# Kernel tuning notes

Hardware: AMD Instinct MI355X
Metric: run time of the kernel (lower is better)

Reference implementation:

```python
import jax, jax.numpy as jnp
import numpy as np

B, DIN, DOUT, E = 131072, 512, 512, 16


def setup_inputs() -> dict:
    key = jax.random.key(0)
    k_x, k_wg, k_we = jax.random.split(key, 3)
    x = jax.random.normal(k_x, (B, DIN), dtype=jnp.float32)
    # gating network params
    Wg = jax.random.normal(k_wg, (DIN, E), dtype=jnp.float32) * 0.02
    bg = jnp.zeros((E,), dtype=jnp.float32)
    # GRN params (torch inits them to zero -> GRN is identity at init)
    gamma = jnp.zeros((E,), dtype=jnp.float32)
    beta = jnp.zeros((E,), dtype=jnp.float32)
    # per-expert linear params, stacked [E, DIN, DOUT]
    We = jax.random.normal(k_we, (E, DIN, DOUT), dtype=jnp.float32) * 0.02
    be = jnp.zeros((E, DOUT), dtype=jnp.float32)
    return {"x": x, "Wg": Wg, "bg": bg, "gamma": gamma, "beta": beta,
            "We": We, "be": be, "topk": 2}


def reference(x, Wg, bg, gamma, beta, We, be, topk):
    # ---- gating: linear -> GRN over expert dim -> softmax ----
    logits = x @ Wg + bg                                   # [B, E]
    Gx = jnp.linalg.norm(logits, axis=1, keepdims=True)    # [B, 1] L2 over experts
    Nx = Gx / (jnp.mean(Gx, axis=0, keepdims=True) + 1e-6) # [B, 1]
    logits = gamma * (logits * Nx) + beta + logits         # GRN residual
    gates = jax.nn.softmax(logits, axis=-1)                # [B, E]
    # ---- top-k routing ----
    top_vals, top_idx = jax.lax.top_k(gates, topk)         # [B, k]
    n_tok = x.shape[0]
    # combine weights scattered back to dense [B, E] (zero for unrouted experts)
    w = jnp.zeros_like(gates).at[jnp.arange(n_tok)[:, None], top_idx].add(top_vals)
    # ---- per-expert linear + weighted combine ----
    out = jnp.zeros((n_tok, We.shape[-1]), dtype=x.dtype)
    for e in range(We.shape[0]):  # small fixed loop over experts
        out = out + w[:, e:e + 1] * (x @ We[e] + be[e])
    return out
```

## Files before the change

kernel.cpp:

```cpp
#include <hip/hip_runtime.h>
#include <hip/hip_bf16.h>
#include <stdint.h>

#define NTOK 131072
#define NE 16

typedef __attribute__((ext_vector_type(8))) short short8;
typedef __attribute__((ext_vector_type(4))) float f32x4;

#define AS1 __attribute__((address_space(1)))
#define AS3 __attribute__((address_space(3)))

__device__ __forceinline__ ushort f2bf(float f) {
    __hip_bfloat16 h = __float2bfloat16(f);
    return *reinterpret_cast<ushort*>(&h);
}


__global__ void k_init(int* ctrl) {
    int tid = threadIdx.x;
    if (tid < 144) ctrl[tid] = 0;
}

__global__ __launch_bounds__(256) void k_wet(const float* __restrict__ We, ushort* __restrict__ WeT) {
    __shared__ float t[64][65];
    int e = blockIdx.z, k0 = blockIdx.x * 64, n0 = blockIdx.y * 64;
    int tid = threadIdx.x;
    const float* src = We + ((size_t)e * 512 + k0) * 512 + n0;
    #pragma unroll
    for (int i = 0; i < 16; i++) {
        int idx = i * 256 + tid;
        int r = idx >> 6, c = idx & 63;
        t[r][c] = src[(size_t)r * 512 + c];
    }
    __syncthreads();
    ushort* dst = WeT + ((size_t)e * 512 + n0) * 512 + k0;
    #pragma unroll
    for (int i = 0; i < 16; i++) {
        int idx = i * 256 + tid;
        int rn = idx >> 6, ck = idx & 63;
        dst[(size_t)rn * 512 + ck] = f2bf(t[ck][rn]);
    }
}

__global__ __launch_bounds__(256) void k_gate(const float* __restrict__ x, const float* __restrict__ Wg,
                                              const float* __restrict__ bg, float* __restrict__ logits,
                                              float* __restrict__ partials, ushort* __restrict__ xbf) {
    __shared__ float WgL[512 * 16];
    __shared__ float xs[256][33];
    __shared__ float wsum[4];
    const int tid = threadIdx.x;
    #pragma unroll
    for (int i = 0; i < 32; i++) WgL[i * 256 + tid] = Wg[i * 256 + tid];
    const size_t tokBase = (size_t)blockIdx.x * 256;
    float acc[16];
    #pragma unroll
    for (int e = 0; e < 16; e++) acc[e] = 0.f;

    for (int kc = 0; kc < 16; kc++) {
        __syncthreads();
        #pragma unroll
        for (int i = 0; i < 8; i++) {
            int idx = (i << 8) + tid;
            int rr = idx >> 3, cq = (idx & 7) << 2;
            const float4 v = *(const float4*)&x[(tokBase + rr) * 512 + (kc << 5) + cq];
            xs[rr][cq] = v.x; xs[rr][cq + 1] = v.y; xs[rr][cq + 2] = v.z; xs[rr][cq + 3] = v.w;
            if (xbf) {
                ushort4 uw;
                uw.x = f2bf(v.x); uw.y = f2bf(v.y); uw.z = f2bf(v.z); uw.w = f2bf(v.w);
                *(ushort4*)&xbf[(tokBase + rr) * 512 + (kc << 5) + cq] = uw;
            }
        }
        __syncthreads();
        #pragma unroll
        for (int j = 0; j < 32; j++) {
            float xv = xs[tid][j];
            const float* wr = &WgL[((kc << 5) + j) << 4];
            #pragma unroll
            for (int e = 0; e < 16; e++) acc[e] = fmaf(xv, wr[e], acc[e]);
        }
    }

    float lg[16];
    float ss = 0.f;
    #pragma unroll
    for (int e = 0; e < 16; e++) {
        float v = acc[e] + bg[e];
        lg[e] = v;
        ss += v * v;
    }
    float gx = sqrtf(ss);
    float r = gx;
    #pragma unroll
    for (int off = 32; off >= 1; off >>= 1) r += __shfl_down(r, off);
    if ((tid & 63) == 0) wsum[tid >> 6] = r;
    __syncthreads();
    if (tid == 0) partials[blockIdx.x] = wsum[0] + wsum[1] + wsum[2] + wsum[3];
    float4* lo = (float4*)(logits + (tokBase + tid) * 16);
    lo[0] = make_float4(lg[0], lg[1], lg[2], lg[3]);
    lo[1] = make_float4(lg[4], lg[5], lg[6], lg[7]);
    lo[2] = make_float4(lg[8], lg[9], lg[10], lg[11]);
    lo[3] = make_float4(lg[12], lg[13], lg[14], lg[15]);
}

__global__ void k_redsum(const float* __restrict__ partials, float* __restrict__ sumGx) {
    int tid = threadIdx.x;
    float s = 0.f;
    #pragma unroll
    for (int i = 0; i < 8; i++) s += partials[tid + i * 64];
    #pragma unroll
    for (int off = 32; off >= 1; off >>= 1) s += __shfl_down(s, off);
    if (tid == 0) *sumGx = s;
}

__global__ __launch_bounds__(256) void k_route(const float* __restrict__ logits, const float* __restrict__ gamma,
                                               const float* __restrict__ beta, const float* __restrict__ sumGx,
                                               int* __restrict__ eP, float2* __restrict__ wP,
                                               int* __restrict__ cnts, int* __restrict__ blockHist) {
    __shared__ int h[32];
    int tid = threadIdx.x;
    if (tid < 32) h[tid] = 0;
    __syncthreads();
    float mean = sumGx[0] * (1.0f / 131072.0f);
    float inv_mean = 1.0f / (mean + 1e-6f);
    #pragma unroll
    for (int it = 0; it < 4; it++) {
        size_t t = (size_t)blockIdx.x * 1024 + it * 256 + tid;
        const float4* lr = (const float4*)(logits + t * 16);
        float4 a0 = lr[0], a1 = lr[1], a2 = lr[2], a3 = lr[3];
        float lg[16] = {a0.x, a0.y, a0.z, a0.w, a1.x, a1.y, a1.z, a1.w,
                        a2.x, a2.y, a2.z, a2.w, a3.x, a3.y, a3.z, a3.w};
        float ss = 0.f;
        #pragma unroll
        for (int e = 0; e < 16; e++) ss += lg[e] * lg[e];
        float nx = sqrtf(ss) * inv_mean;
        #pragma unroll
        for (int e = 0; e < 16; e++) lg[e] = gamma[e] * (lg[e] * nx) + beta[e] + lg[e];
        int e1 = 0; float v1 = lg[0];
        #pragma unroll
        for (int e = 1; e < 16; e++) if (lg[e] > v1) { v1 = lg[e]; e1 = e; }
        int e2 = -1; float v2 = -3.4e38f;
        #pragma unroll
        for (int e = 0; e < 16; e++) if (e != e1 && lg[e] > v2) { v2 = lg[e]; e2 = e; }
        float s = 0.f;
        #pragma unroll
        for (int e = 0; e < 16; e++) s += expf(lg[e] - v1);
        float w1 = 1.0f / s;
        float w2 = expf(v2 - v1) / s;
        eP[t] = e1 | (e2 << 8);
        wP[t] = make_float2(w1, w2);
        atomicAdd(&h[e1], 1);
        atomicAdd(&h[16 + e2], 1);
    }
    __syncthreads();
    if (tid < 32) {
        atomicAdd(&cnts[tid], h[tid]);
        blockHist[blockIdx.x * 32 + tid] = h[tid];
    }
}

__global__ void k_scan(int* ctrl, int* blockHist) {
    int t = threadIdx.x;
    if (t < 32) {
        int run = 0;
        for (int b = 0; b < 128; b++) {
            int v = blockHist[b * 32 + t];
            blockHist[b * 32 + t] = run;
            run += v;
        }
    }
    __syncthreads();
    if (t == 0) {
        int s = 0;
        for (int e = 0; e < 16; e++) { ctrl[64 + e] = s; s += ctrl[e]; }
        s = 0;
        for (int e = 0; e < 16; e++) { ctrl[80 + e] = s; s += ctrl[16 + e]; }
        int tt = 0; ctrl[96] = 0;
        for (int e = 0; e < 16; e++) { tt += (ctrl[e] + 63) >> 6; ctrl[96 + e + 1] = tt; }
        tt = 0; ctrl[113] = 0;
        for (int e = 0; e < 16; e++) { tt += (ctrl[16 + e] + 63) >> 6; ctrl[113 + e + 1] = tt; }
    }
}

__global__ __launch_bounds__(256) void k_scatter(const int* __restrict__ eP, const float2* __restrict__ wP,
                                                 const int* __restrict__ ctrl, const int* __restrict__ blockHist,
                                                 int* __restrict__ listA, float* __restrict__ wA,
                                                 int* __restrict__ listB, float* __restrict__ wB) {
    __shared__ int waveCnt[4][32];
    __shared__ int runCnt[32];
    const int tid = threadIdx.x;
    const int lane = tid & 63;
    const int wv = tid >> 6;
    if (tid < 32) runCnt[tid] = blockHist[blockIdx.x * 32 + tid];
    __syncthreads();
    const unsigned long long below = (1ull << lane) - 1ull;
    for (int it = 0; it < 4; it++) {
        size_t t = (size_t)blockIdx.x * 1024 + it * 256 + tid;
        int ep = eP[t];
        float2 w = wP[t];
        int e1 = ep & 255, e2 = (ep >> 8) & 255;
        int r1 = 0, r2 = 0;
        for (int e = 0; e < 16; e++) {
            unsigned long long m1 = __ballot(e1 == e);
            unsigned long long m2 = __ballot(e2 == e);
            if (e1 == e) r1 = __popcll(m1 & below);
            if (e2 == e) r2 = __popcll(m2 & below);
            if (lane == e) {
                waveCnt[wv][e] = __popcll(m1);
                waveCnt[wv][16 + e] = __popcll(m2);
            }
        }
        __syncthreads();
        if (tid < 32) {
            int s = runCnt[tid];
            #pragma unroll
            for (int ww = 0; ww < 4; ww++) { int v = waveCnt[ww][tid]; waveCnt[ww][tid] = s; s += v; }
            runCnt[tid] = s;
        }
        __syncthreads();
        int i1 = ctrl[64 + e1] + waveCnt[wv][e1] + r1;
        listA[i1] = (int)t; wA[i1] = w.x;
        int i2 = ctrl[80 + e2] + waveCnt[wv][16 + e2] + r2;
        listB[i2] = (int)t; wB[i2] = w.y;
        __syncthreads();
    }
}

template <int ADD, int ABF>
__global__ __launch_bounds__(256, 3) void k_gemm(const float* __restrict__ x, const ushort* __restrict__ xbf,
                                                 const ushort* __restrict__ WeT,
                                                 const float* __restrict__ be,
                                                 const int* __restrict__ list, const float* __restrict__ wlist,
                                                 const int* __restrict__ cnts, const int* __restrict__ offs,
                                                 const int* __restrict__ tileOff,
                                                 float* __restrict__ out) {
    __shared__ ushort lds[20480];
    const int tid = threadIdx.x;
    const int q = (int)gridDim.x >> 3;
    const int bid = ((int)blockIdx.x & 7) * q + ((int)blockIdx.x >> 3);
    const int ry = bid >> 1;
    const int nh = bid & 1;
    if (ry >= tileOff[16]) return;
    int e = 0;
    #pragma unroll
    for (int i = 1; i < 16; i++) if (ry >= tileOff[i]) e = i;
    const int cnt = cnts[e];
    const int off = offs[e];
    const int rowStart = (ry - tileOff[e]) << 6;
    const int n0 = nh << 8;

    const int sRow = tid >> 2, sQ = tid & 3;
    const int gRow = rowStart + sRow;
    const int tokS = (gRow < cnt) ? list[off + gRow] : 0;
    const float* xrowF = x + (size_t)tokS * 512 + sQ * 16;
    const ushort* xrowH = xbf + (size_t)tokS * 512 + sQ * 16;
    const int aswz = (sRow & 7) << 4;
    const int awr0 = 32768 + sRow * 128;

    const char* weB = (const char*)WeT + (size_t)e * 524288 + (size_t)n0 * 1024;

    const int lane = tid & 63;
    const int wid = tid >> 6;
    const int wN = wid << 6;
    const int l16 = lane & 15;
    const int lq = lane >> 4;
    const int mswz = (l16 & 7) << 4;
    const int kbL = lq << 4;

    f32x4 acc[4][4];
    f32x4 zero = {0.f, 0.f, 0.f, 0.f};
    #pragma unroll
    for (int i = 0; i < 4; i++)
        #pragma unroll
        for (int j = 0; j < 4; j++) acc[i][j] = zero;

    auto stageB = [&](int kt) {
        #pragma unroll
        for (int i = 0; i < 8; i++) {
            int D = (tid << 4) + (i << 12);
            int nr = D >> 7, inner = D & 127;
            int sb = inner ^ ((nr & 7) << 4);
            const char* gp = weB + nr * 1024 + kt * 128 + sb;
            __builtin_amdgcn_global_load_lds((const AS1 void*)gp, (AS3 void*)&lds[D >> 1], 16, 0, 0);
        }
    };
    float4 vaF[4];
    short8 vaH[2];
    auto loadA = [&](int kt) {
        if (ABF) {
            const short8* xp = (const short8*)(xrowH + kt * 64);
            vaH[0] = xp[0]; vaH[1] = xp[1];
        } else {
            const float4* xp = (const float4*)(xrowF + kt * 64);
            #pragma unroll
            for (int j = 0; j < 4; j++) vaF[j] = xp[j];
        }
    };
    auto writeA = [&]() {
        #pragma unroll
        for (int h = 0; h < 2; h++) {
            int db = awr0 + (((sQ << 5) + (h << 4)) ^ aswz);
            if (ABF) {
                *(short8*)((char*)lds + db) = vaH[h];
            } else {
                alignas(16) ushort tw[8];
                float4 p = vaF[h * 2], q2 = vaF[h * 2 + 1];
                tw[0] = f2bf(p.x); tw[1] = f2bf(p.y); tw[2] = f2bf(p.z); tw[3] = f2bf(p.w);
                tw[4] = f2bf(q2.x); tw[5] = f2bf(q2.y); tw[6] = f2bf(q2.z); tw[7] = f2bf(q2.w);
                *(short8*)((char*)lds + db) = *(const short8*)tw;
            }
        }
    };
    auto compute = [&]() {
        #pragma unroll
        for (int ks = 0; ks < 2; ks++) {
            const int kb = (ks << 6) + kbL;
            short8 af[4], bfr[4];
            #pragma unroll
            for (int mf = 0; mf < 4; mf++) {
                int m = (mf << 4) + l16;
                af[mf] = *(const short8*)((const char*)lds + 32768 + (m << 7) + (kb ^ mswz));
            }
            #pragma unroll
            for (int nf = 0; nf < 4; nf++) {
                int n = wN + (nf << 4) + l16;
                bfr[nf] = *(const short8*)((const char*)lds + (n << 7) + (kb ^ mswz));
            }
            #pragma unroll
            for (int mf = 0; mf < 4; mf++)
                #pragma unroll
                for (int nf = 0; nf < 4; nf++)
                    acc[mf][nf] = __builtin_amdgcn_mfma_f32_16x16x32_bf16(af[mf], bfr[nf], acc[mf][nf], 0, 0, 0);
        }
    };

    loadA(0);
    #pragma unroll
    for (int kt = 0; kt < 8; kt++) {
        __syncthreads();
        stageB(kt);
        writeA();
        if (kt < 7) loadA(kt + 1);
        __syncthreads();
        compute();
    }

    float bias[4];
    #pragma unroll
    for (int nf = 0; nf < 4; nf++) bias[nf] = be[e * 512 + n0 + wN + (nf << 4) + l16];
    float* lsf = (float*)lds;
    __syncthreads();
    #pragma unroll
    for (int mf = 0; mf < 4; mf++) {
        int rb = rowStart + (mf << 4) + (lq << 2);
        #pragma unroll
        for (int i = 0; i < 4; i++) {
            int r = rb + i;
            float wv_ = (r < cnt) ? wlist[off + r] : 0.f;
            int lrow = (lq << 2) + i;
            #pragma unroll
            for (int nf = 0; nf < 4; nf++)
                lsf[lrow * 260 + wN + (nf << 4) + l16] = wv_ * (acc[mf][nf][i] + bias[nf]);
        }
        __syncthreads();
        {
            int lrow = tid >> 4, seg = tid & 15;
            int r = rowStart + (mf << 4) + lrow;
            if (r < cnt) {
                int tok = list[off + r];
                float* orow = out + (size_t)tok * 512 + n0;
                #pragma unroll
                for (int j = 0; j < 4; j++) {
                    int c = (seg << 2) + (j << 6);
                    float4 v = *(float4*)&lsf[lrow * 260 + c];
                    if (ADD) {
                        float4 o = *(const float4*)&orow[c];
                        v.x += o.x; v.y += o.y; v.z += o.z; v.w += o.w;
                    }
                    *(float4*)&orow[c] = v;
                }
            }
        }
        __syncthreads();
    }
}

extern "C" void kernel_launch(void* const* d_in, const int* in_sizes, int n_in,
                              void* d_out, int out_size, void* d_ws, size_t ws_size,
                              hipStream_t stream) {
    const float* x = (const float*)d_in[0];
    const float* Wg = (const float*)d_in[1];
    const float* bg = (const float*)d_in[2];
    const float* gamma = (const float*)d_in[3];
    const float* beta = (const float*)d_in[4];
    const float* We = (const float*)d_in[5];
    const float* be = (const float*)d_in[6];
    float* out = (float*)d_out;
    char* ws = (char*)d_ws;

    ushort* WeT = (ushort*)(ws);
    float* logits = (float*)(ws + 8388608);
    int* listA = (int*)(ws + 16777216);
    float* wA = (float*)(ws + 17301504);
    int* listB = (int*)(ws + 17825792);
    float* wB = (float*)(ws + 18350080);
    int* eP = (int*)(ws + 18874368);
    float2* wP = (float2*)(ws + 19398656);
    int* ctrl = (int*)(ws + 20447232);
    int* blockHist = (int*)(ws + 20451328);
    float* ctrlF = (float*)ctrl;
    float* partials = (float*)(ws + 16777216);

    const size_t XBF_OFF = 20480000;
    const size_t XBF_BYTES = (size_t)NTOK * 512 * 2;
    bool useBF = (ws_size >= XBF_OFF + XBF_BYTES);
    ushort* xbf = useBF ? (ushort*)(ws + XBF_OFF) : nullptr;

    k_init<<<1, 256, 0, stream>>>(ctrl);
    k_wet<<<dim3(8, 8, 16), 256, 0, stream>>>(We, WeT);
    k_gate<<<512, 256, 0, stream>>>(x, Wg, bg, logits, partials, xbf);
    k_redsum<<<1, 64, 0, stream>>>(partials, ctrlF + 130);
    k_route<<<128, 256, 0, stream>>>(logits, gamma, beta, ctrlF + 130, eP, wP, ctrl, blockHist);
    k_scan<<<1, 64, 0, stream>>>(ctrl, blockHist);
    k_scatter<<<128, 256, 0, stream>>>(eP, wP, ctrl, blockHist, listA, wA, listB, wB);
    if (useBF) {
        k_gemm<0, 1><<<4160, 256, 0, stream>>>(x, xbf, WeT, be, listA, wA, ctrl, ctrl + 64, ctrl + 96, out);
        k_gemm<1, 1><<<4160, 256, 0, stream>>>(x, xbf, WeT, be, listB, wB, ctrl + 16, ctrl + 80, ctrl + 113, out);
    } else {
        k_gemm<0, 0><<<4160, 256, 0, stream>>>(x, xbf, WeT, be, listA, wA, ctrl, ctrl + 64, ctrl + 96, out);
        k_gemm<1, 0><<<4160, 256, 0, stream>>>(x, xbf, WeT, be, listB, wB, ctrl + 16, ctrl + 80, ctrl + 113, out);
    }
}
```

Measured before the change: 481.9 us.

## Pre-swizzle expert weights into MFMA fragment order and load B directly to registers

```diff
diff --git a/kernel.cpp b/kernel.cpp
--- a/kernel.cpp
+++ b/kernel.cpp
@@ -8,9 +8,6 @@
 typedef __attribute__((ext_vector_type(8))) short short8;
 typedef __attribute__((ext_vector_type(4))) float f32x4;
 
-#define AS1 __attribute__((address_space(1)))
-#define AS3 __attribute__((address_space(3)))
-
 __device__ __forceinline__ ushort f2bf(float f) {
     __hip_bfloat16 h = __float2bfloat16(f);
     return *reinterpret_cast<ushort*>(&h);
@@ -22,7 +19,7 @@
     if (tid < 144) ctrl[tid] = 0;
 }
 
-__global__ __launch_bounds__(256) void k_wet(const float* __restrict__ We, ushort* __restrict__ WeT) {
+__global__ __launch_bounds__(256) void k_wet(const float* __restrict__ We, ushort* __restrict__ WeTF) {
     __shared__ float t[64][65];
     int e = blockIdx.z, k0 = blockIdx.x * 64, n0 = blockIdx.y * 64;
     int tid = threadIdx.x;
@@ -34,12 +31,23 @@
         t[r][c] = src[(size_t)r * 512 + c];
     }
     __syncthreads();
-    ushort* dst = WeT + ((size_t)e * 512 + n0) * 512 + k0;
-    #pragma unroll
-    for (int i = 0; i < 16; i++) {
-        int idx = i * 256 + tid;
-        int rn = idx >> 6, ck = idx & 63;
-        dst[(size_t)rn * 512 + ck] = f2bf(t[ck][rn]);
+    #pragma unroll
+    for (int i = 0; i < 2; i++) {
+        int u = i * 256 + tid;
+        int ktl = u >> 8;
+        int ntl = (u >> 6) & 3;
+        int lane = u & 63;
+        int l16 = lane & 15, lq = lane >> 4;
+        alignas(16) ushort tw[8];
+        #pragma unroll
+        for (int j = 0; j < 8; j++) {
+            int kl = ktl * 32 + lq * 8 + j;
+            int nl = ntl * 16 + l16;
+            tw[j] = f2bf(t[kl][nl]);
+        }
+        size_t o = (size_t)e * 262144 + (size_t)((n0 >> 4) + ntl) * 8192
+                 + (size_t)((k0 >> 5) + ktl) * 512 + lane * 8;
+        *(short8*)(WeTF + o) = *(const short8*)tw;
     }
 }
 
@@ -228,13 +236,13 @@
 
 template <int ADD, int ABF>
 __global__ __launch_bounds__(256, 3) void k_gemm(const float* __restrict__ x, const ushort* __restrict__ xbf,
-                                                 const ushort* __restrict__ WeT,
+                                                 const ushort* __restrict__ WeTF,
                                                  const float* __restrict__ be,
                                                  const int* __restrict__ list, const float* __restrict__ wlist,
                                                  const int* __restrict__ cnts, const int* __restrict__ offs,
                                                  const int* __restrict__ tileOff,
                                                  float* __restrict__ out) {
-    __shared__ ushort lds[20480];
+    __shared__ alignas(16) ushort lds[10240];
     const int tid = threadIdx.x;
     const int q = (int)gridDim.x >> 3;
     const int bid = ((int)blockIdx.x & 7) * q + ((int)blockIdx.x >> 3);
@@ -255,9 +263,7 @@
     const float* xrowF = x + (size_t)tokS * 512 + sQ * 16;
     const ushort* xrowH = xbf + (size_t)tokS * 512 + sQ * 16;
     const int aswz = (sRow & 7) << 4;
-    const int awr0 = 32768 + sRow * 128;
-
-    const char* weB = (const char*)WeT + (size_t)e * 524288 + (size_t)n0 * 1024;
+    const int awr0 = sRow * 128;
 
     const int lane = tid & 63;
     const int wid = tid >> 6;
@@ -267,6 +273,8 @@
     const int mswz = (l16 & 7) << 4;
     const int kbL = lq << 4;
 
+    const ushort* bp = WeTF + (size_t)e * 262144 + (size_t)((n0 + wN) >> 4) * 8192 + lane * 8;
+
     f32x4 acc[4][4];
     f32x4 zero = {0.f, 0.f, 0.f, 0.f};
     #pragma unroll
@@ -274,15 +282,10 @@
         #pragma unroll
         for (int j = 0; j < 4; j++) acc[i][j] = zero;
 
-    auto stageB = [&](int kt) {
-        #pragma unroll
-        for (int i = 0; i < 8; i++) {
-            int D = (tid << 4) + (i << 12);
-            int nr = D >> 7, inner = D & 127;
-            int sb = inner ^ ((nr & 7) << 4);
-            const char* gp = weB + nr * 1024 + kt * 128 + sb;
-            __builtin_amdgcn_global_load_lds((const AS1 void*)gp, (AS3 void*)&lds[D >> 1], 16, 0, 0);
-        }
+    short8 bE[4], bO[4];
+    auto loadB = [&](int hs, short8* b) {
+        #pragma unroll
+        for (int nf = 0; nf < 4; nf++) b[nf] = *(const short8*)(bp + nf * 8192 + hs * 512);
     };
     float4 vaF[4];
     short8 vaH[2];
@@ -296,10 +299,10 @@
             for (int j = 0; j < 4; j++) vaF[j] = xp[j];
         }
     };
-    auto writeA = [&]() {
+    auto writeA = [&](int buf) {
         #pragma unroll
         for (int h = 0; h < 2; h++) {
-            int db = awr0 + (((sQ << 5) + (h << 4)) ^ aswz);
+            int db = awr0 + buf * 8192 + (((sQ << 5) + (h << 4)) ^ aswz);
             if (ABF) {
                 *(short8*)((char*)lds + db) = vaH[h];
             } else {
@@ -311,38 +314,39 @@
             }
         }
     };
-    auto compute = [&]() {
-        #pragma unroll
-        for (int ks = 0; ks < 2; ks++) {
-            const int kb = (ks << 6) + kbL;
-            short8 af[4], bfr[4];
+    auto computeHS = [&](int buf, int ks, short8* b) {
+        const int kb = (ks << 6) + kbL;
+        short8 af[4];
+        #pragma unroll
+        for (int mf = 0; mf < 4; mf++) {
+            int m = (mf << 4) + l16;
+            af[mf] = *(const short8*)((const char*)lds + buf * 8192 + (m << 7) + (kb ^ mswz));
+        }
+        #pragma unroll
+        for (int mf = 0; mf < 4; mf++)
             #pragma unroll
-            for (int mf = 0; mf < 4; mf++) {
-                int m = (mf << 4) + l16;
-                af[mf] = *(const short8*)((const char*)lds + 32768 + (m << 7) + (kb ^ mswz));
-            }
-            #pragma unroll
-            for (int nf = 0; nf < 4; nf++) {
-                int n = wN + (nf << 4) + l16;
-                bfr[nf] = *(const short8*)((const char*)lds + (n << 7) + (kb ^ mswz));
-            }
-            #pragma unroll
-            for (int mf = 0; mf < 4; mf++)
-                #pragma unroll
-                for (int nf = 0; nf < 4; nf++)
-                    acc[mf][nf] = __builtin_amdgcn_mfma_f32_16x16x32_bf16(af[mf], bfr[nf], acc[mf][nf], 0, 0, 0);
-        }
+            for (int nf = 0; nf < 4; nf++)
+                acc[mf][nf] = __builtin_amdgcn_mfma_f32_16x16x32_bf16(af[mf], b[nf], acc[mf][nf], 0, 0, 0);
     };
 
     loadA(0);
+    writeA(0);
+    loadA(1);
+    loadB(0, bE);
+    __syncthreads();
+
     #pragma unroll
     for (int kt = 0; kt < 8; kt++) {
-        __syncthreads();
-        stageB(kt);
-        writeA();
-        if (kt < 7) loadA(kt + 1);
-        __syncthreads();
-        compute();
+        const int buf = kt & 1;
+        loadB(2 * kt + 1, bO);
+        computeHS(buf, 0, bE);
+        if (kt < 7) {
+            loadB(2 * kt + 2, bE);
+            writeA(buf ^ 1);
+            if (kt < 6) loadA(kt + 2);
+        }
+        computeHS(buf, 1, bO);
+        __syncthreads();
     }
 
     float bias[4];
@@ -398,7 +402,7 @@
     float* out = (float*)d_out;
     char* ws = (char*)d_ws;
 
-    ushort* WeT = (ushort*)(ws);
+    ushort* WeTF = (ushort*)(ws);
     float* logits = (float*)(ws + 8388608);
     int* listA = (int*)(ws + 16777216);
     float* wA = (float*)(ws + 17301504);
@@ -417,17 +421,17 @@
     ushort* xbf = useBF ? (ushort*)(ws + XBF_OFF) : nullptr;
 
     k_init<<<1, 256, 0, stream>>>(ctrl);
-    k_wet<<<dim3(8, 8, 16), 256, 0, stream>>>(We, WeT);
+    k_wet<<<dim3(8, 8, 16), 256, 0, stream>>>(We, WeTF);
     k_gate<<<512, 256, 0, stream>>>(x, Wg, bg, logits, partials, xbf);
     k_redsum<<<1, 64, 0, stream>>>(partials, ctrlF + 130);
     k_route<<<128, 256, 0, stream>>>(logits, gamma, beta, ctrlF + 130, eP, wP, ctrl, blockHist);
     k_scan<<<1, 64, 0, stream>>>(ctrl, blockHist);
     k_scatter<<<128, 256, 0, stream>>>(eP, wP, ctrl, blockHist, listA, wA, listB, wB);
     if (useBF) {
-        k_gemm<0, 1><<<4160, 256, 0, stream>>>(x, xbf, WeT, be, listA, wA, ctrl, ctrl + 64, ctrl + 96, out);
-        k_gemm<1, 1><<<4160, 256, 0, stream>>>(x, xbf, WeT, be, listB, wB, ctrl + 16, ctrl + 80, ctrl + 113, out);
+        k_gemm<0, 1><<<4160, 256, 0, stream>>>(x, xbf, WeTF, be, listA, wA, ctrl, ctrl + 64, ctrl + 96, out);
+        k_gemm<1, 1><<<4160, 256, 0, stream>>>(x, xbf, WeTF, be, listB, wB, ctrl + 16, ctrl + 80, ctrl + 113, out);
     } else {
-        k_gemm<0, 0><<<4160, 256, 0, stream>>>(x, xbf, WeT, be, listA, wA, ctrl, ctrl + 64, ctrl + 96, out);
-        k_gemm<1, 0><<<4160, 256, 0, stream>>>(x, xbf, WeT, be, listB, wB, ctrl + 16, ctrl + 80, ctrl + 113, out);
-    }
-}
+        k_gemm<0, 0><<<4160, 256, 0, stream>>>(x, xbf, WeTF, be, listA, wA, ctrl, ctrl + 64, ctrl + 96, out);
+        k_gemm<1, 0><<<4160, 256, 0, stream>>>(x, xbf, WeTF, be, listB, wB, ctrl + 16, ctrl + 80, ctrl + 113, out);
+    }
+}
```

Result: slower. 514.9 us (+6.8%).
